# Kernel tuning notes

Measured on AMD Instinct MI355X. Metric: run time of the kernel, lower is better.

## Reference

```python
import jax, jax.numpy as jnp
import numpy as np

B, H, S, D = 4, 16, 2048, 64

def setup_inputs() -> dict:
    key = jax.random.key(0)
    kq, kk, kv = jax.random.split(key, 3)
    q = jax.random.normal(kq, (B, H, S, D), dtype=jnp.float32)
    k = jax.random.normal(kk, (B, H, S, D), dtype=jnp.float32)
    v = jax.random.normal(kv, (B, H, S, D), dtype=jnp.float32)
    # causal mask: True where attention is DISALLOWED (masked_fill semantics)
    row = jnp.arange(S)[:, None]
    col = jnp.arange(S)[None, :]
    attn_mask = (col > row)[None, None, :, :]  # [1,1,S,S] bool
    return {"q": q, "k": k, "v": v, "attn_mask": attn_mask}

def reference(q, k, v, attn_mask):
    scale = 1.0 / jnp.sqrt(jnp.float32(q.shape[-1]))
    # [B,H,S,S] scores
    scores = jnp.einsum("bhqd,bhkd->bhqk", q, k) * scale
    scores = jnp.where(attn_mask, -jnp.inf, scores)
    attn = jax.nn.softmax(scores, axis=-1)
    # dropout p=0 (eval) -> identity
    context = jnp.einsum("bhqk,bhkd->bhqd", attn, v)
    return context
```

## Files before the change

### kernel.cpp

```cpp
#include <hip/hip_runtime.h>

#define BB 4
#define HH 16
#define SS 2048
#define DD 64
#define NTILE (SS / 64)
#define BLOB_U16 8192

typedef __bf16 bf16x8 __attribute__((ext_vector_type(8)));
typedef __bf16 bf16x2 __attribute__((ext_vector_type(2)));
typedef float  f32x4  __attribute__((ext_vector_type(4)));
typedef unsigned short u16;
typedef unsigned int   u32;
typedef unsigned int   u32x2 __attribute__((ext_vector_type(2)));

__device__ __forceinline__ u16 f2bf(float f) {
    u32 u = __float_as_uint(f);
    u = (u + 0x7fffu + ((u >> 16) & 1u)) >> 16;
    return (u16)u;
}

__device__ __forceinline__ u32 pack2bf(float a, float b) {
#if __has_builtin(__builtin_amdgcn_cvt_pk_bf16_f32)
    bf16x2 t = __builtin_amdgcn_cvt_pk_bf16_f32(a, b);
    return __builtin_bit_cast(u32, t);
#else
    return (u32)f2bf(a) | ((u32)f2bf(b) << 16);
#endif
}

__device__ __forceinline__ u32x2 pl32(u32 a, u32 b) {
#if __has_builtin(__builtin_amdgcn_permlane32_swap)
    return __builtin_amdgcn_permlane32_swap(a, b, false, false);
#else
    asm("v_permlane32_swap_b32 %0, %1" : "+v"(a), "+v"(b));
    u32x2 r; r.x = a; r.y = b; return r;
#endif
}
__device__ __forceinline__ u32x2 pl16(u32 a, u32 b) {
#if __has_builtin(__builtin_amdgcn_permlane16_swap)
    return __builtin_amdgcn_permlane16_swap(a, b, false, false);
#else
    asm("v_permlane16_swap_b32 %0, %1" : "+v"(a), "+v"(b));
    u32x2 r; r.x = a; r.y = b; return r;
#endif
}

__device__ __forceinline__ void dma16(const void* g, const void* l) {
    __builtin_amdgcn_global_load_lds(
        (const __attribute__((address_space(1))) void*)g,
        (__attribute__((address_space(3))) void*)l, 16, 0, 0);
}

__global__ void prep(const float* __restrict__ k, const float* __restrict__ v,
                     u16* __restrict__ ws)
{
    __shared__ u16 tile[64 * 68];
    const int bh = blockIdx.y, ti = blockIdx.x, tid = threadIdx.x;
    const size_t ibase = (size_t)bh * SS * DD + (size_t)ti * 64 * DD;
    u16* blob = ws + (size_t)(bh * NTILE + ti) * BLOB_U16;

    {
        const float4* ks4 = (const float4*)(k + ibase) + tid * 4;
        union { u16 h[16]; uint4 u[2]; } ok;
        #pragma unroll
        for (int j = 0; j < 4; ++j) {
            float4 b = ks4[j];
            ok.h[j*4+0] = f2bf(b.x); ok.h[j*4+1] = f2bf(b.y);
            ok.h[j*4+2] = f2bf(b.z); ok.h[j*4+3] = f2bf(b.w);
        }
        const int r  = tid >> 2;
        const int c2 = (tid & 3) * 2;
        u16* kd = blob + r * 64;
        *(uint4*)(kd + ((c2    ) ^ (r & 7)) * 8) = ok.u[0];
        *(uint4*)(kd + ((c2 + 1) ^ (r & 7)) * 8) = ok.u[1];
    }
    {
        const int s4 = (tid >> 4) * 4;
        const int d4 = (tid & 15) * 4;
        float4 r0 = *(const float4*)(v + ibase + (size_t)(s4 + 0) * DD + d4);
        float4 r1 = *(const float4*)(v + ibase + (size_t)(s4 + 1) * DD + d4);
        float4 r2 = *(const float4*)(v + ibase + (size_t)(s4 + 2) * DD + d4);
        float4 r3 = *(const float4*)(v + ibase + (size_t)(s4 + 3) * DD + d4);
        const float c0[4] = {r0.x, r0.y, r0.z, r0.w};
        const float c1[4] = {r1.x, r1.y, r1.z, r1.w};
        const float c2[4] = {r2.x, r2.y, r2.z, r2.w};
        const float c3[4] = {r3.x, r3.y, r3.z, r3.w};
        #pragma unroll
        for (int i = 0; i < 4; ++i) {
            uint2 o;
            o.x = pack2bf(c0[i], c1[i]);
            o.y = pack2bf(c2[i], c3[i]);
            *(uint2*)(&tile[(d4 + i) * 68 + s4]) = o;
        }
    }
    __syncthreads();
    const int d  = tid >> 2;
    const int ch = tid & 3;
    uint4 o0 = *(const uint4*)(&tile[d * 68 + ch * 16]);
    uint4 o1 = *(const uint4*)(&tile[d * 68 + ch * 16 + 8]);
    u16* vd = blob + 4096 + d * 64;
    *(uint4*)(vd + ((ch * 2    ) ^ (d & 7)) * 8) = o0;
    *(uint4*)(vd + ((ch * 2 + 1) ^ (d & 7)) * 8) = o1;
}

template<bool DOU>
__device__ __forceinline__ void fa_tile(
    const char* __restrict__ Bb, const int kv0,
    const bf16x8 (&qf)[2][2],
    const int s0L, const int s0U,
    const int m16, const int quad, const int offA0, const int offA1,
    const bf16x8 ones,
    f32x4 (&accL)[4], f32x4 (&accU)[4], f32x4 &laccL, f32x4 &laccU)
{
    const f32x4 vzero = {0.f, 0.f, 0.f, 0.f};
    u32 ppL[4][2], ppU[4][2];
    #pragma unroll
    for (int st = 0; st < 4; ++st) {
        const bf16x8 kf0 = *(const bf16x8*)(Bb + st * 2048 + offA0);
        const bf16x8 kf1 = *(const bf16x8*)(Bb + st * 2048 + offA1);
        {
            f32x4 s = __builtin_amdgcn_mfma_f32_16x16x32_bf16(
                kf0, qf[0][0], vzero, 0, 0, 0);
            s = __builtin_amdgcn_mfma_f32_16x16x32_bf16(
                kf1, qf[0][1], s, 0, 0, 0);
            if (kv0 + 63 > s0L) {
                const int qq = s0L + m16;
                const int kb = kv0 + st * 16 + quad * 4;
                #pragma unroll
                for (int r = 0; r < 4; ++r)
                    if (kb + r > qq) s[r] = -1e30f;
            }
            const float p0 = __builtin_exp2f(s[0]);
            const float p1 = __builtin_exp2f(s[1]);
            const float p2 = __builtin_exp2f(s[2]);
            const float p3 = __builtin_exp2f(s[3]);
            ppL[st][0] = pack2bf(p0, p1);
            ppL[st][1] = pack2bf(p2, p3);
        }
        if (DOU) {
            f32x4 s = __builtin_amdgcn_mfma_f32_16x16x32_bf16(
                kf0, qf[1][0], vzero, 0, 0, 0);
            s = __builtin_amdgcn_mfma_f32_16x16x32_bf16(
                kf1, qf[1][1], s, 0, 0, 0);
            if (kv0 + 63 > s0U) {
                const int qq = s0U + m16;
                const int kb = kv0 + st * 16 + quad * 4;
                #pragma unroll
                for (int r = 0; r < 4; ++r)
                    if (kb + r > qq) s[r] = -1e30f;
            }
            const float p0 = __builtin_exp2f(s[0]);
            const float p1 = __builtin_exp2f(s[1]);
            const float p2 = __builtin_exp2f(s[2]);
            const float p3 = __builtin_exp2f(s[3]);
            ppU[st][0] = pack2bf(p0, p1);
            ppU[st][1] = pack2bf(p2, p3);
        }
    }
    bf16x8 pfL[2], pfU[2];
    #pragma unroll
    for (int kc = 0; kc < 2; ++kc) {
        u32x2 t0 = pl32(ppL[2 * kc][0], ppL[2 * kc + 1][0]);
        u32x2 r0 = pl16(t0.x, t0.y);
        u32x2 t1 = pl32(ppL[2 * kc][1], ppL[2 * kc + 1][1]);
        u32x2 r1 = pl16(t1.x, t1.y);
        union { u32 u[4]; bf16x8 v; } pfu;
        pfu.u[0] = r0.x; pfu.u[1] = r1.x;
        pfu.u[2] = r0.y; pfu.u[3] = r1.y;
        pfL[kc] = pfu.v;
    }
    if (DOU) {
        #pragma unroll
        for (int kc = 0; kc < 2; ++kc) {
            u32x2 t0 = pl32(ppU[2 * kc][0], ppU[2 * kc + 1][0]);
            u32x2 r0 = pl16(t0.x, t0.y);
            u32x2 t1 = pl32(ppU[2 * kc][1], ppU[2 * kc + 1][1]);
            u32x2 r1 = pl16(t1.x, t1.y);
            union { u32 u[4]; bf16x8 v; } pfu;
            pfu.u[0] = r0.x; pfu.u[1] = r1.x;
            pfu.u[2] = r0.y; pfu.u[3] = r1.y;
            pfU[kc] = pfu.v;
        }
    }
    laccL = __builtin_amdgcn_mfma_f32_16x16x32_bf16(ones, pfL[0], laccL, 0, 0, 0);
    laccL = __builtin_amdgcn_mfma_f32_16x16x32_bf16(ones, pfL[1], laccL, 0, 0, 0);
    if (DOU) {
        laccU = __builtin_amdgcn_mfma_f32_16x16x32_bf16(ones, pfU[0], laccU, 0, 0, 0);
        laccU = __builtin_amdgcn_mfma_f32_16x16x32_bf16(ones, pfU[1], laccU, 0, 0, 0);
    }
    #pragma unroll
    for (int dt = 0; dt < 4; ++dt) {
        const bf16x8 vf0 = *(const bf16x8*)(Bb + 8192 + dt * 2048 + offA0);
        const bf16x8 vf1 = *(const bf16x8*)(Bb + 8192 + dt * 2048 + offA1);
        accL[dt] = __builtin_amdgcn_mfma_f32_16x16x32_bf16(
            vf0, pfL[0], accL[dt], 0, 0, 0);
        accL[dt] = __builtin_amdgcn_mfma_f32_16x16x32_bf16(
            vf1, pfL[1], accL[dt], 0, 0, 0);
        if (DOU) {
            accU[dt] = __builtin_amdgcn_mfma_f32_16x16x32_bf16(
                vf0, pfU[0], accU[dt], 0, 0, 0);
            accU[dt] = __builtin_amdgcn_mfma_f32_16x16x32_bf16(
                vf1, pfU[1], accU[dt], 0, 0, 0);
        }
    }
}

__global__ __launch_bounds__(512, 4) void fa3(
    const float* __restrict__ q, const u16* __restrict__ ws,
    float* __restrict__ out)
{
    const int tid  = threadIdx.x;
    const int lane = tid & 63;
    const int w    = tid >> 6;
    const int quad = lane >> 4;
    const int m16  = lane & 15;
    const int bx   = blockIdx.x;
    const int rr   = bx >> 8;
    const int jj   = (bx >> 6) & 3;
    const int bh   = bx & 63;
    const int a    = rr ? (7 - jj) : jj;
    const size_t base = (size_t)bh * SS * DD;
    const int s0U = a * 128 + w * 16;
    const int s0L = (15 - a) * 128 + w * 16;

    __shared__ __align__(16) u16 KV[2 * BLOB_U16];

    const int swz   = (m16 & 7) << 4;
    const int offA0 = m16 * 128 + ((quad * 16) ^ swz);
    const int offA1 = m16 * 128 + ((quad * 16 + 64) ^ swz);

    const float qsc = 0.18033688011112042f;
    bf16x8 qf[2][2];
    #pragma unroll
    for (int sx = 0; sx < 2; ++sx) {
        const int s0 = sx ? s0U : s0L;
        #pragma unroll
        for (int dc = 0; dc < 2; ++dc) {
            const float* qp = q + base + (size_t)(s0 + m16) * DD
                              + dc * 32 + quad * 8;
            float4 fa = *(const float4*)(qp);
            float4 fb = *(const float4*)(qp + 4);
            union { u32 u[4]; bf16x8 v; } t;
            t.u[0] = pack2bf(fa.x * qsc, fa.y * qsc);
            t.u[1] = pack2bf(fa.z * qsc, fa.w * qsc);
            t.u[2] = pack2bf(fb.x * qsc, fb.y * qsc);
            t.u[3] = pack2bf(fb.z * qsc, fb.w * qsc);
            qf[sx][dc] = t.v;
        }
    }

    const f32x4 vzero = {0.f, 0.f, 0.f, 0.f};
    f32x4 accL[4], accU[4], laccL = vzero, laccU = vzero;
    #pragma unroll
    for (int dt = 0; dt < 4; ++dt) { accL[dt] = vzero; accU[dt] = vzero; }

    union { u32 u[4]; bf16x8 v; } onesu;
    onesu.u[0] = 0x3F803F80u; onesu.u[1] = 0x3F803F80u;
    onesu.u[2] = 0x3F803F80u; onesu.u[3] = 0x3F803F80u;
    const bf16x8 ones = onesu.v;

    const int ntiles = 32 - 2 * a;
    const char* gsrcT = (const char*)ws + (size_t)bh * NTILE * 16384
                        + (size_t)tid * 16;

    {
        u16* l = KV + tid * 8;
        dma16(gsrcT, l);
        dma16(gsrcT + 8192, l + 4096);
    }

    for (int t = 0; t < ntiles; ++t) {
        const int kv0 = t * 64;
        asm volatile("s_waitcnt vmcnt(0)" ::: "memory");
        __syncthreads();
        const char* Bb = (const char*)KV + (t & 1) * 16384;

        if (t + 1 < ntiles) {
            const char* g = gsrcT + (size_t)(t + 1) * 16384;
            u16* l = KV + ((t + 1) & 1) * BLOB_U16 + tid * 8;
            dma16(g, l);
            dma16(g + 8192, l + 4096);
        }

        const bool doL = (kv0 <= s0L + 15);
        const bool doU = (kv0 <= s0U + 15);
        if (doL) {
            if (doU)
                fa_tile<true >(Bb, kv0, qf, s0L, s0U, m16, quad, offA0, offA1,
                               ones, accL, accU, laccL, laccU);
            else
                fa_tile<false>(Bb, kv0, qf, s0L, s0U, m16, quad, offA0, offA1,
                               ones, accL, accU, laccL, laccU);
        }
    }

    {
        const float inv = 1.f / laccL[0];
        const int qq = s0L + m16;
        #pragma unroll
        for (int dt = 0; dt < 4; ++dt) {
            float4 o = make_float4(accL[dt][0] * inv, accL[dt][1] * inv,
                                   accL[dt][2] * inv, accL[dt][3] * inv);
            *(float4*)(out + base + (size_t)qq * DD + dt * 16 + quad * 4) = o;
        }
    }
    {
        const float inv = 1.f / laccU[0];
        const int qq = s0U + m16;
        #pragma unroll
        for (int dt = 0; dt < 4; ++dt) {
            float4 o = make_float4(accU[dt][0] * inv, accU[dt][1] * inv,
                                   accU[dt][2] * inv, accU[dt][3] * inv);
            *(float4*)(out + base + (size_t)qq * DD + dt * 16 + quad * 4) = o;
        }
    }
}

extern "C" void kernel_launch(void* const* d_in, const int* in_sizes, int n_in,
                              void* d_out, int out_size, void* d_ws, size_t ws_size,
                              hipStream_t stream)
{
    const float* q = (const float*)d_in[0];
    const float* k = (const float*)d_in[1];
    const float* v = (const float*)d_in[2];
    float* out = (float*)d_out;

    u16* ws = (u16*)d_ws;

    prep<<<dim3(NTILE, BB * HH), dim3(256), 0, stream>>>(k, v, ws);
    fa3<<<dim3(8 * 64), dim3(512), 0, stream>>>(q, ws, out);
}
```

Before: 210.4 us.

## Fuse K/V bf16 conversion into attention kernel, dropping prep pass

Removes the separate prep kernel that converted K and V to swizzled bf16 blobs in a workspace. The attention kernel now loads fp32 K/V into registers, converts them and writes them transposed and swizzled into LDS, software-pipelined so the next tile's loads overlap the current tile's compute. This saves a kernel launch and the workspace write/read round trip. In exchange it adds register pressure, more global fp32 traffic because each block re-reads and re-converts the same K/V, and it drops the async global-to-LDS DMA path.

```diff
diff --git a/kernel.cpp b/kernel.cpp
--- a/kernel.cpp
+++ b/kernel.cpp
@@ -4,29 +4,17 @@
 #define HH 16
 #define SS 2048
 #define DD 64
-#define NTILE (SS / 64)
-#define BLOB_U16 8192
 
 typedef __bf16 bf16x8 __attribute__((ext_vector_type(8)));
-typedef __bf16 bf16x2 __attribute__((ext_vector_type(2)));
 typedef float  f32x4  __attribute__((ext_vector_type(4)));
 typedef unsigned short u16;
 typedef unsigned int   u32;
 typedef unsigned int   u32x2 __attribute__((ext_vector_type(2)));
 
-__device__ __forceinline__ u16 f2bf(float f) {
-    u32 u = __float_as_uint(f);
-    u = (u + 0x7fffu + ((u >> 16) & 1u)) >> 16;
-    return (u16)u;
-}
-
 __device__ __forceinline__ u32 pack2bf(float a, float b) {
-#if __has_builtin(__builtin_amdgcn_cvt_pk_bf16_f32)
-    bf16x2 t = __builtin_amdgcn_cvt_pk_bf16_f32(a, b);
-    return __builtin_bit_cast(u32, t);
-#else
-    return (u32)f2bf(a) | ((u32)f2bf(b) << 16);
-#endif
+    u32 r;
+    asm("v_cvt_pk_bf16_f32 %0, %1, %2" : "=v"(r) : "v"(a), "v"(b));
+    return r;
 }
 
 __device__ __forceinline__ u32x2 pl32(u32 a, u32 b) {
@@ -44,64 +32,6 @@
     asm("v_permlane16_swap_b32 %0, %1" : "+v"(a), "+v"(b));
     u32x2 r; r.x = a; r.y = b; return r;
 #endif
-}
-
-__device__ __forceinline__ void dma16(const void* g, const void* l) {
-    __builtin_amdgcn_global_load_lds(
-        (const __attribute__((address_space(1))) void*)g,
-        (__attribute__((address_space(3))) void*)l, 16, 0, 0);
-}
-
-__global__ void prep(const float* __restrict__ k, const float* __restrict__ v,
-                     u16* __restrict__ ws)
-{
-    __shared__ u16 tile[64 * 68];
-    const int bh = blockIdx.y, ti = blockIdx.x, tid = threadIdx.x;
-    const size_t ibase = (size_t)bh * SS * DD + (size_t)ti * 64 * DD;
-    u16* blob = ws + (size_t)(bh * NTILE + ti) * BLOB_U16;
-
-    {
-        const float4* ks4 = (const float4*)(k + ibase) + tid * 4;
-        union { u16 h[16]; uint4 u[2]; } ok;
-        #pragma unroll
-        for (int j = 0; j < 4; ++j) {
-            float4 b = ks4[j];
-            ok.h[j*4+0] = f2bf(b.x); ok.h[j*4+1] = f2bf(b.y);
-            ok.h[j*4+2] = f2bf(b.z); ok.h[j*4+3] = f2bf(b.w);
-        }
-        const int r  = tid >> 2;
-        const int c2 = (tid & 3) * 2;
-        u16* kd = blob + r * 64;
-        *(uint4*)(kd + ((c2    ) ^ (r & 7)) * 8) = ok.u[0];
-        *(uint4*)(kd + ((c2 + 1) ^ (r & 7)) * 8) = ok.u[1];
-    }
-    {
-        const int s4 = (tid >> 4) * 4;
-        const int d4 = (tid & 15) * 4;
-        float4 r0 = *(const float4*)(v + ibase + (size_t)(s4 + 0) * DD + d4);
-        float4 r1 = *(const float4*)(v + ibase + (size_t)(s4 + 1) * DD + d4);
-        float4 r2 = *(const float4*)(v + ibase + (size_t)(s4 + 2) * DD + d4);
-        float4 r3 = *(const float4*)(v + ibase + (size_t)(s4 + 3) * DD + d4);
-        const float c0[4] = {r0.x, r0.y, r0.z, r0.w};
-        const float c1[4] = {r1.x, r1.y, r1.z, r1.w};
-        const float c2[4] = {r2.x, r2.y, r2.z, r2.w};
-        const float c3[4] = {r3.x, r3.y, r3.z, r3.w};
-        #pragma unroll
-        for (int i = 0; i < 4; ++i) {
-            uint2 o;
-            o.x = pack2bf(c0[i], c1[i]);
-            o.y = pack2bf(c2[i], c3[i]);
-            *(uint2*)(&tile[(d4 + i) * 68 + s4]) = o;
-        }
-    }
-    __syncthreads();
-    const int d  = tid >> 2;
-    const int ch = tid & 3;
-    uint4 o0 = *(const uint4*)(&tile[d * 68 + ch * 16]);
-    uint4 o1 = *(const uint4*)(&tile[d * 68 + ch * 16 + 8]);
-    u16* vd = blob + 4096 + d * 64;
-    *(uint4*)(vd + ((ch * 2    ) ^ (d & 7)) * 8) = o0;
-    *(uint4*)(vd + ((ch * 2 + 1) ^ (d & 7)) * 8) = o1;
 }
 
 template<bool DOU>
@@ -207,8 +137,8 @@
 }
 
 __global__ __launch_bounds__(512, 4) void fa3(
-    const float* __restrict__ q, const u16* __restrict__ ws,
-    float* __restrict__ out)
+    const float* __restrict__ q, const float* __restrict__ kg,
+    const float* __restrict__ vg, float* __restrict__ out)
 {
     const int tid  = threadIdx.x;
     const int lane = tid & 63;
@@ -224,7 +154,16 @@
     const int s0U = a * 128 + w * 16;
     const int s0L = (15 - a) * 128 + w * 16;
 
-    __shared__ __align__(16) u16 KV[2 * BLOB_U16];
+    __shared__ __align__(16) u16 KV[2][8192];
+
+    const bool isK = (tid < 256);
+    const int  h   = tid & 255;
+    const int  kr  = h >> 2;
+    const int  kc  = h & 3;
+    const int  vs4 = (h >> 4) * 4;
+    const int  vd4 = (h & 15) * 4;
+    const float* gK = kg + base + (size_t)kr * DD + kc * 16;
+    const float* gV = vg + base + (size_t)vs4 * DD + vd4;
 
     const int swz   = (m16 & 7) << 4;
     const int offA0 = m16 * 128 + ((quad * 16) ^ swz);
@@ -261,27 +200,60 @@
     const bf16x8 ones = onesu.v;
 
     const int ntiles = 32 - 2 * a;
-    const char* gsrcT = (const char*)ws + (size_t)bh * NTILE * 16384
-                        + (size_t)tid * 16;
+
+    auto gload = [&](int tt, float4& x0, float4& x1, float4& x2, float4& x3) {
+        if (isK) {
+            const float4* p = (const float4*)(gK + (size_t)tt * 4096);
+            x0 = p[0]; x1 = p[1]; x2 = p[2]; x3 = p[3];
+        } else {
+            const float* p = gV + (size_t)tt * 4096;
+            x0 = *(const float4*)(p);
+            x1 = *(const float4*)(p + DD);
+            x2 = *(const float4*)(p + 2 * DD);
+            x3 = *(const float4*)(p + 3 * DD);
+        }
+    };
+    auto cvt_write = [&](int buf, float4 x0, float4 x1, float4 x2, float4 x3) {
+        if (isK) {
+            uint4 A, B;
+            A.x = pack2bf(x0.x, x0.y); A.y = pack2bf(x0.z, x0.w);
+            A.z = pack2bf(x1.x, x1.y); A.w = pack2bf(x1.z, x1.w);
+            B.x = pack2bf(x2.x, x2.y); B.y = pack2bf(x2.z, x2.w);
+            B.z = pack2bf(x3.x, x3.y); B.w = pack2bf(x3.z, x3.w);
+            u16* kd = &KV[buf][kr * 64];
+            *(uint4*)(kd + (((2 * kc)     ^ (kr & 7)) << 3)) = A;
+            *(uint4*)(kd + (((2 * kc + 1) ^ (kr & 7)) << 3)) = B;
+        } else {
+            const float c0[4] = {x0.x, x0.y, x0.z, x0.w};
+            const float c1[4] = {x1.x, x1.y, x1.z, x1.w};
+            const float c2[4] = {x2.x, x2.y, x2.z, x2.w};
+            const float c3[4] = {x3.x, x3.y, x3.z, x3.w};
+            #pragma unroll
+            for (int j = 0; j < 4; ++j) {
+                uint2 o;
+                o.x = pack2bf(c0[j], c1[j]);
+                o.y = pack2bf(c2[j], c3[j]);
+                const int row = vd4 + j;
+                *(uint2*)(&KV[buf][4096 + row * 64 +
+                    (((vs4 >> 3) ^ (row & 7)) << 3) + (vs4 & 4)]) = o;
+            }
+        }
+    };
 
     {
-        u16* l = KV + tid * 8;
-        dma16(gsrcT, l);
-        dma16(gsrcT + 8192, l + 4096);
+        float4 x0, x1, x2, x3;
+        gload(0, x0, x1, x2, x3);
+        cvt_write(0, x0, x1, x2, x3);
     }
 
     for (int t = 0; t < ntiles; ++t) {
+        __syncthreads();
         const int kv0 = t * 64;
-        asm volatile("s_waitcnt vmcnt(0)" ::: "memory");
-        __syncthreads();
-        const char* Bb = (const char*)KV + (t & 1) * 16384;
-
-        if (t + 1 < ntiles) {
-            const char* g = gsrcT + (size_t)(t + 1) * 16384;
-            u16* l = KV + ((t + 1) & 1) * BLOB_U16 + tid * 8;
-            dma16(g, l);
-            dma16(g + 8192, l + 4096);
-        }
+        const char* Bb = (const char*)&KV[t & 1][0];
+
+        float4 x0, x1, x2, x3;
+        const bool hn = (t + 1 < ntiles);
+        if (hn) gload(t + 1, x0, x1, x2, x3);
 
         const bool doL = (kv0 <= s0L + 15);
         const bool doU = (kv0 <= s0U + 15);
@@ -293,6 +265,8 @@
                 fa_tile<false>(Bb, kv0, qf, s0L, s0U, m16, quad, offA0, offA1,
                                ones, accL, accU, laccL, laccU);
         }
+
+        if (hn) cvt_write((t + 1) & 1, x0, x1, x2, x3);
     }
 
     {
@@ -325,9 +299,7 @@
     const float* k = (const float*)d_in[1];
     const float* v = (const float*)d_in[2];
     float* out = (float*)d_out;
-
-    u16* ws = (u16*)d_ws;
-
-    prep<<<dim3(NTILE, BB * HH), dim3(256), 0, stream>>>(k, v, ws);
-    fa3<<<dim3(8 * 64), dim3(512), 0, stream>>>(q, ws, out);
-}
+    (void)d_ws; (void)ws_size;
+
+    fa3<<<dim3(8 * 64), dim3(512), 0, stream>>>(q, k, v, out);
+}
```

Result: faster. 195.9 us (-6.9%).
